# Kernel tuning notes

Measured on AMD Instinct MI355X. Metric: run time of the kernel, lower is better.

## Reference

```python
import jax, jax.numpy as jnp
import numpy as np

D = 2048
H = 16
DK = D // H
B = 2
S = 2048


def setup_inputs() -> dict:
    key = jax.random.key(0)
    ks = jax.random.split(key, 11)
    s = 1.0 / np.sqrt(D)
    inp = {
        "q": jax.random.normal(ks[0], (B, S, D), jnp.float32),
        "k": jax.random.normal(ks[1], (B, S, D), jnp.float32),
        "v": jax.random.normal(ks[2], (B, S, D), jnp.float32),
        "mask": 0,
        "Wq": jax.random.normal(ks[3], (D, D), jnp.float32) * s,
        "bq": jax.random.normal(ks[4], (D,), jnp.float32) * s,
        "Wk": jax.random.normal(ks[5], (D, D), jnp.float32) * s,
        "bk": jax.random.normal(ks[6], (D,), jnp.float32) * s,
        "Wv": jax.random.normal(ks[7], (D, D), jnp.float32) * s,
        "bv": jax.random.normal(ks[8], (D,), jnp.float32) * s,
        "Wo": jax.random.normal(ks[9], (D, D), jnp.float32) * s,
        "bo": jax.random.normal(ks[10], (D,), jnp.float32) * s,
    }
    return inp


def reference(q, k, v, mask, Wq, bq, Wk, bk, Wv, bv, Wo, bo):
    # Linear projections (torch Linear: x @ W.T + b)
    query = q @ Wq.T + bq  # [B,S,D]
    key_ = k @ Wk.T + bk
    value = v @ Wv.T + bv
    # split heads -> [B,S,H,DK]
    query = query.reshape(B, S, H, DK)
    key_ = key_.reshape(B, S, H, DK)
    value = value.reshape(B, S, H, DK)
    # scores [B,H,Sq,Sk]
    scores = jnp.einsum('nqhd,nkhd->nhqk', query, key_)
    if mask:
        # faithful to source: fill where triu(ones, diag=1) == 0 (lower tri incl diag)
        tri = jnp.triu(jnp.ones((S, S), jnp.float32), k=1)
        scores = jnp.where(tri == 0, jnp.float32(-1e20), scores)
    attn = jax.nn.softmax(scores / np.sqrt(DK), axis=3)
    # dropout=0.0 -> identity
    out = jnp.einsum('nhql,nlhd->nqhd', attn, value).reshape(B, S, D)
    return out @ Wo.T + bo
```

## Files before the change

kernel.cpp:

```cpp
#include <hip/hip_runtime.h>
#include <math.h>

typedef unsigned short u16;
typedef u16 u16x8 __attribute__((ext_vector_type(8)));
typedef u16 u16x4 __attribute__((ext_vector_type(4)));
typedef short s16x8 __attribute__((ext_vector_type(8)));
typedef short s16x4 __attribute__((ext_vector_type(4)));
typedef float f32x4 __attribute__((ext_vector_type(4)));

static constexpr int B_ = 2;
static constexpr int S_ = 2048;
static constexpr int D_ = 2048;
static constexpr int H_ = 16;
static constexpr int DK = 128;
static constexpr long long BSD = (long long)B_ * S_ * D_;
static constexpr long long DD  = (long long)D_ * D_;

#if __has_builtin(__builtin_amdgcn_mfma_f32_16x16x32_bf16)
#define HAVE_MFMA32 1
#else
#define HAVE_MFMA32 0
#endif
#if __has_builtin(__builtin_amdgcn_mfma_f32_16x16x16bf16_1k)
#define HAVE_MFMA16 1
#else
#define HAVE_MFMA16 0
#endif

__device__ __forceinline__ u16 f2bf(float f) {
    union { float f; unsigned u; } cv; cv.f = f;
    unsigned u = cv.u;
    return (u16)((u + 0x7fffu + ((u >> 16) & 1u)) >> 16);
}

__device__ __forceinline__ unsigned pack2bf(float a, float b) {
    union { float f; unsigned u; } x, y; x.f = a; y.f = b;
    return ((y.u + 0x8000u) & 0xffff0000u) | ((x.u + 0x8000u) >> 16);
}

__device__ __forceinline__ f32x4 mfma32(f32x4 c, u16x8 a, u16x8 b) {
#if HAVE_MFMA32
    return __builtin_amdgcn_mfma_f32_16x16x32_bf16((s16x8)a, (s16x8)b, c, 0, 0, 0);
#else
    asm volatile("v_mfma_f32_16x16x32_bf16 %0, %1, %2, %0" : "+v"(c) : "v"(a), "v"(b));
    return c;
#endif
}
__device__ __forceinline__ f32x4 mfma16(f32x4 c, u16x4 a, u16x4 b) {
#if HAVE_MFMA16
    return __builtin_amdgcn_mfma_f32_16x16x16bf16_1k((s16x4)a, (s16x4)b, c, 0, 0, 0);
#else
    asm volatile("v_mfma_f32_16x16x16_bf16 %0, %1, %2, %0" : "+v"(c) : "v"(a), "v"(b));
    return c;
#endif
}
__device__ __forceinline__ void fence32() {
#if !HAVE_MFMA32
    asm volatile("s_nop 7\ns_nop 7" :::);
#endif
}
__device__ __forceinline__ void fence16() {
#if !HAVE_MFMA16
    asm volatile("s_nop 7\ns_nop 7" :::);
#endif
}

__device__ __forceinline__ void glds16(const u16* g, u16* l) {
    __builtin_amdgcn_global_load_lds(
        (const __attribute__((address_space(1))) unsigned int*)g,
        (__attribute__((address_space(3))) unsigned int*)l, 16, 0, 0);
}

__device__ __forceinline__ float fexp2(float x) {
#if __has_builtin(__builtin_amdgcn_exp2f)
    return __builtin_amdgcn_exp2f(x);
#else
    return exp2f(x);
#endif
}

struct CastArgs {
    const float* src[7];
    u16* dst[7];
    int start[8];
};
__global__ __launch_bounds__(256) void cast_all(CastArgs a) {
    int g = blockIdx.x * 256 + threadIdx.x;
    if (g >= a.start[7]) return;
    int seg = 0;
#pragma unroll
    for (int i = 1; i < 7; ++i) seg += (g >= a.start[i]) ? 1 : 0;
    int idx = g - a.start[seg];
    float4 f = ((const float4*)a.src[seg])[idx];
    ushort4 o;
    o.x = f2bf(f.x); o.y = f2bf(f.y); o.z = f2bf(f.z); o.w = f2bf(f.w);
    ((ushort4*)a.dst[seg])[idx] = o;
}

__global__ __launch_bounds__(256) void transpose_v(const u16* __restrict__ V,
                                                   u16* __restrict__ Vt) {
    __shared__ u16 tile[32][33];
    int z = blockIdx.z;
    int b = z >> 4, h = z & 15;
    const u16* src = V + (long long)b * S_ * D_ + (long long)h * DK;
    u16* dst = Vt + (long long)z * DK * S_;
    int l0 = blockIdx.x * 32, d0 = blockIdx.y * 32;
    int c = threadIdx.x & 31, r0 = threadIdx.x >> 5;
#pragma unroll
    for (int i = 0; i < 4; ++i) {
        int r = r0 + i * 8;
        tile[r][c] = src[(long long)(l0 + r) * D_ + d0 + c];
    }
    __syncthreads();
#pragma unroll
    for (int i = 0; i < 4; ++i) {
        int r = r0 + i * 8;
        dst[(long long)(d0 + r) * S_ + l0 + c] = tile[c][r];
    }
}

template <typename OutT, bool BIAS>
__global__ __launch_bounds__(256) void gemm_bt(const u16* __restrict__ A,
                                               const u16* __restrict__ B,
                                               OutT* __restrict__ C,
                                               const float* __restrict__ bias,
                                               float scale) {
    __shared__ u16 SM[8192];
    u16* As = SM;
    u16* Bs = SM + 4096;

    const int t = threadIdx.x;
    const int wave = t >> 6, lane = t & 63;
    const int quad = lane >> 4, l16 = lane & 15;
    const int wm = (wave >> 1) * 64;
    const int wn = (wave & 1) * 64;
    const long long m0 = (long long)blockIdx.y * 128;
    const long long n0 = (long long)blockIdx.x * 128;

    f32x4 acc[4][4];
#pragma unroll
    for (int i = 0; i < 4; ++i)
#pragma unroll
        for (int j = 0; j < 4; ++j)
            acc[i][j] = f32x4{0.f, 0.f, 0.f, 0.f};

    for (int k0 = 0; k0 < D_; k0 += 32) {
        __syncthreads();
#pragma unroll
        for (int s = 0; s < 2; ++s) {
            int slot = s * 256 + t;
            int row = slot >> 2;
            int c = (t & 3) ^ ((row >> 1) & 3);
            glds16(A + (m0 + row) * D_ + k0 + c * 8, &As[slot * 8]);
        }
#pragma unroll
        for (int s = 0; s < 2; ++s) {
            int slot = s * 256 + t;
            int row = slot >> 2;
            int c = (t & 3) ^ ((row >> 1) & 3);
            glds16(B + (n0 + row) * D_ + k0 + c * 8, &Bs[slot * 8]);
        }
        __syncthreads();

        u16x8 af[4], bf[4];
#pragma unroll
        for (int i = 0; i < 4; ++i) {
            int row = wm + i * 16 + l16;
            af[i] = *(const u16x8*)(&As[row * 32 + ((quad ^ ((row >> 1) & 3)) * 8)]);
        }
#pragma unroll
        for (int j = 0; j < 4; ++j) {
            int row = wn + j * 16 + l16;
            bf[j] = *(const u16x8*)(&Bs[row * 32 + ((quad ^ ((row >> 1) & 3)) * 8)]);
        }
#pragma unroll
        for (int i = 0; i < 4; ++i)
#pragma unroll
            for (int j = 0; j < 4; ++j)
                acc[i][j] = mfma32(acc[i][j], af[i], bf[j]);
    }

    fence32();

    float bs[4];
#pragma unroll
    for (int j = 0; j < 4; ++j)
        bs[j] = BIAS ? bias[(int)n0 + wn + j * 16 + l16] : 0.f;

    if constexpr (sizeof(OutT) == 2) {
#pragma unroll
        for (int p = 0; p < 2; ++p) {
            __syncthreads();
#pragma unroll
            for (int jj = 0; jj < 2; ++jj) {
                int j = p * 2 + jj;
#pragma unroll
                for (int i = 0; i < 4; ++i)
#pragma unroll
                    for (int r = 0; r < 4; ++r) {
                        int row = wm + i * 16 + quad * 4 + r;
                        int lc = (wave & 1) * 32 + jj * 16 + l16;
                        SM[row * 64 + lc] = f2bf((acc[i][j][r] + bs[j]) * scale);
                    }
            }
            __syncthreads();
#pragma unroll
            for (int i = 0; i < 4; ++i) {
                int idx = i * 256 + t;
                int row = idx >> 3, cc = idx & 7;
                u16x8 val = *(const u16x8*)(&SM[row * 64 + cc * 8]);
                long long n = n0 + 32 * p + (cc & 3) * 8 + (cc >> 2) * 64;
                *(u16x8*)((u16*)C + (m0 + row) * (long long)D_ + n) = val;
            }
        }
    } else {
        float* Cf = (float*)SM;
#pragma unroll
        for (int p = 0; p < 4; ++p) {
            __syncthreads();
            int j = p;
#pragma unroll
            for (int i = 0; i < 4; ++i)
#pragma unroll
                for (int r = 0; r < 4; ++r) {
                    int row = wm + i * 16 + quad * 4 + r;
                    int lc = (wave & 1) * 16 + l16;
                    Cf[row * 32 + lc] = (acc[i][j][r] + bs[j]) * scale;
                }
            __syncthreads();
#pragma unroll
            for (int i = 0; i < 4; ++i) {
                int idx = i * 256 + t;
                int row = idx >> 3, cc = idx & 7;
                f32x4 val = *(const f32x4*)(&Cf[row * 32 + cc * 4]);
                long long n = n0 + 16 * p + (cc & 3) * 4 + (cc >> 2) * 64;
                *(f32x4*)((float*)C + (m0 + row) * (long long)D_ + n) = val;
            }
        }
    }
}

__global__ __launch_bounds__(512, 2) void flash_attn(const u16* __restrict__ Qb,
                                                     const u16* __restrict__ Kb,
                                                     const u16* __restrict__ Vt,
                                                     u16* __restrict__ Ob) {
    extern __shared__ u16 SM[];
    const int z  = blockIdx.x;
    const int qt = blockIdx.y;
    const int b  = z >> 4, h = z & 15;
    const int t = threadIdx.x, wave = t >> 6, lane = t & 63;
    const int quad = lane >> 4, l16 = lane & 15;

    u16* Ksb0 = SM;
    u16* Ksb1 = SM + 16384;
    u16* Vsb0 = SM + 32768;
    u16* Vsb1 = SM + 49152;

    const u16* kbase = Kb + (long long)(b * S_) * D_ + h * DK;
    const u16* vbase = Vt + (long long)z * DK * S_;

    u16x8 qf[2][4];
    {
        const u16* qbase = Qb + ((long long)(b * S_ + qt * 256 + wave * 32 + l16)) * D_
                              + h * DK + quad * 8;
#pragma unroll
        for (int jq = 0; jq < 2; ++jq)
#pragma unroll
            for (int kk = 0; kk < 4; ++kk)
                qf[jq][kk] = *(const u16x8*)(qbase + (long long)jq * 16 * D_ + kk * 32);
    }

    f32x4 acc_o[2][8];
#pragma unroll
    for (int jq = 0; jq < 2; ++jq)
#pragma unroll
        for (int jd = 0; jd < 8; ++jd)
            acc_o[jq][jd] = f32x4{0.f, 0.f, 0.f, 0.f};
    float m_[2] = {-3e38f, -3e38f}, l_[2] = {0.f, 0.f};

    {
#pragma unroll
        for (int i = 0; i < 4; ++i) {
            int slot = i * 512 + t;
            int row = slot >> 4;
            int cs = (slot & 15) ^ (row & 7);
            glds16(kbase + (long long)row * D_ + cs * 8, Ksb0 + slot * 8);
        }
#pragma unroll
        for (int i = 0; i < 4; ++i) {
            int slot = i * 512 + t;
            int row = slot >> 4;
            int cs = (slot & 15) ^ (row & 7);
            glds16(vbase + (long long)row * S_ + cs * 8, Vsb0 + slot * 8);
        }
    }

    for (int kt = 0; kt < S_ / 128; ++kt) {
        __syncthreads();
        const int p = kt & 1;
        const u16* ks = p ? Ksb1 : Ksb0;
        const u16* vs = p ? Vsb1 : Vsb0;
        if (kt + 1 < S_ / 128) {
            u16* kd = p ? Ksb0 : Ksb1;
            u16* vd = p ? Vsb0 : Vsb1;
            const u16* ksrc = kbase + (long long)(kt + 1) * 128 * D_;
            const u16* vsrc = vbase + (kt + 1) * 128;
#pragma unroll
            for (int i = 0; i < 4; ++i) {
                int slot = i * 512 + t;
                int row = slot >> 4;
                int cs = (slot & 15) ^ (row & 7);
                glds16(ksrc + (long long)row * D_ + cs * 8, kd + slot * 8);
            }
#pragma unroll
            for (int i = 0; i < 4; ++i) {
                int slot = i * 512 + t;
                int row = slot >> 4;
                int cs = (slot & 15) ^ (row & 7);
                glds16(vsrc + (long long)row * S_ + cs * 8, vd + slot * 8);
            }
        }

        f32x4 st[8][2];
#pragma unroll
        for (int ik = 0; ik < 8; ++ik)
#pragma unroll
            for (int jq = 0; jq < 2; ++jq)
                st[ik][jq] = f32x4{0.f, 0.f, 0.f, 0.f};
#pragma unroll
        for (int kk = 0; kk < 4; ++kk) {
            u16x8 kf[8];
#pragma unroll
            for (int ik = 0; ik < 8; ++ik) {
                int krow = ik * 16 + l16;
                kf[ik] = *(const u16x8*)(&ks[krow * 128 + (((kk * 4 + quad) ^ (l16 & 7)) * 8)]);
            }
#pragma unroll
            for (int ik = 0; ik < 8; ++ik) {
                st[ik][0] = mfma32(st[ik][0], kf[ik], qf[0][kk]);
                st[ik][1] = mfma32(st[ik][1], kf[ik], qf[1][kk]);
            }
        }
        fence32();

        float alpha[2];
#pragma unroll
        for (int jq = 0; jq < 2; ++jq) {
            float mx = st[0][jq][0];
#pragma unroll
            for (int ik = 0; ik < 8; ++ik)
#pragma unroll
                for (int r = 0; r < 4; ++r) mx = fmaxf(mx, st[ik][jq][r]);
            mx = fmaxf(mx, __shfl_xor(mx, 16, 64));
            mx = fmaxf(mx, __shfl_xor(mx, 32, 64));
            float mn = fmaxf(m_[jq], mx);
            alpha[jq] = fexp2(m_[jq] - mn);
            m_[jq] = mn;
            float sum = 0.f;
#pragma unroll
            for (int ik = 0; ik < 8; ++ik)
#pragma unroll
                for (int r = 0; r < 4; ++r) {
                    float pv = fexp2(st[ik][jq][r] - mn);
                    st[ik][jq][r] = pv;
                    sum += pv;
                }
            sum += __shfl_xor(sum, 16, 64);
            sum += __shfl_xor(sum, 32, 64);
            l_[jq] = l_[jq] * alpha[jq] + sum;
        }

        float ar[2][4];
#pragma unroll
        for (int jq = 0; jq < 2; ++jq)
#pragma unroll
            for (int r = 0; r < 4; ++r)
                ar[jq][r] = __shfl(alpha[jq], quad * 20 + r, 64);
#pragma unroll
        for (int jq = 0; jq < 2; ++jq)
#pragma unroll
            for (int jd = 0; jd < 8; ++jd)
#pragma unroll
                for (int r = 0; r < 4; ++r)
                    acc_o[jq][jd][r] *= ar[jq][r];

#pragma unroll
        for (int ik = 0; ik < 8; ++ik) {
            u16x4 pf0, pf1;
            {
                union { u16x4 v; unsigned u[2]; } pk;
                pk.u[0] = pack2bf(st[ik][0][0], st[ik][0][1]);
                pk.u[1] = pack2bf(st[ik][0][2], st[ik][0][3]);
                pf0 = pk.v;
                pk.u[0] = pack2bf(st[ik][1][0], st[ik][1][1]);
                pk.u[1] = pack2bf(st[ik][1][2], st[ik][1][3]);
                pf1 = pk.v;
            }
            const int kc = ik * 4 + quad;
            const int chi = kc >> 1, clo = kc & 1;
            u16x4 vf[8];
#pragma unroll
            for (int jd = 0; jd < 8; ++jd) {
                int vrow = jd * 16 + l16;
                vf[jd] = *(const u16x4*)(&vs[vrow * 128 + ((chi ^ (l16 & 7)) * 8) + clo * 4]);
            }
#pragma unroll
            for (int jd = 0; jd < 8; ++jd) {
                acc_o[0][jd] = mfma16(acc_o[0][jd], pf0, vf[jd]);
                acc_o[1][jd] = mfma16(acc_o[1][jd], pf1, vf[jd]);
            }
        }
        fence16();
    }

    float lr[2][4];
#pragma unroll
    for (int jq = 0; jq < 2; ++jq) {
        float inv = 1.f / l_[jq];
#pragma unroll
        for (int r = 0; r < 4; ++r)
            lr[jq][r] = __shfl(inv, quad * 20 + r, 64);
    }
    __syncthreads();
#pragma unroll
    for (int jq = 0; jq < 2; ++jq)
#pragma unroll
        for (int r = 0; r < 4; ++r) {
            int qloc = wave * 32 + jq * 16 + quad * 4 + r;
#pragma unroll
            for (int jd = 0; jd < 8; ++jd)
                SM[qloc * 128 + jd * 16 + l16] = f2bf(acc_o[jq][jd][r] * lr[jq][r]);
        }
    __syncthreads();
    u16* obase = Ob + ((long long)(b * S_ + qt * 256)) * D_ + h * DK;
#pragma unroll
    for (int i = 0; i < 8; ++i) {
        int idx = i * 512 + t;
        int row = idx >> 4, cc = idx & 15;
        *(u16x8*)(obase + (long long)row * D_ + cc * 8) = *(const u16x8*)(&SM[row * 128 + cc * 8]);
    }
}

extern "C" void kernel_launch(void* const* d_in, const int* in_sizes, int n_in,
                              void* d_out, int out_size, void* d_ws, size_t ws_size,
                              hipStream_t stream) {
    const float* q  = (const float*)d_in[0];
    const float* k  = (const float*)d_in[1];
    const float* v  = (const float*)d_in[2];
    const float* Wq = (const float*)d_in[4];
    const float* bq = (const float*)d_in[5];
    const float* Wk = (const float*)d_in[6];
    const float* bk = (const float*)d_in[7];
    const float* Wv = (const float*)d_in[8];
    const float* bv = (const float*)d_in[9];
    const float* Wo = (const float*)d_in[10];
    const float* bo = (const float*)d_in[11];
    float* out = (float*)d_out;

    u16* ws = (u16*)d_ws;
    u16* xq  = ws; ws += BSD;
    u16* xk  = ws; ws += BSD;
    u16* xv  = ws; ws += BSD;
    u16* wqb = ws; ws += DD;
    u16* wkb = ws; ws += DD;
    u16* wvb = ws; ws += DD;
    u16* wob = ws; ws += DD;
    u16* Qb  = ws; ws += BSD;
    u16* Kb  = ws; ws += BSD;
    u16* Vb  = ws; ws += BSD;
    u16* Vt  = ws; ws += BSD;
    u16* Ob  = ws; ws += BSD;

    const float q_scale = (float)(0.08838834764831845 * 1.4426950408889634);

    {
        CastArgs a;
        const float* srcs[7] = {q, k, v, Wq, Wk, Wv, Wo};
        u16* dsts[7] = {xq, xk, xv, wqb, wkb, wvb, wob};
        int n4s[7] = {(int)(BSD / 4), (int)(BSD / 4), (int)(BSD / 4),
                      (int)(DD / 4), (int)(DD / 4), (int)(DD / 4), (int)(DD / 4)};
        int acc = 0;
        for (int i = 0; i < 7; ++i) { a.src[i] = srcs[i]; a.dst[i] = dsts[i]; a.start[i] = acc; acc += n4s[i]; }
        a.start[7] = acc;
        cast_all<<<(acc + 255) / 256, 256, 0, stream>>>(a);
    }

    {
        dim3 g(D_ / 128, (B_ * S_) / 128);
        gemm_bt<u16, true><<<g, 256, 0, stream>>>(xq, wqb, Qb, bq, q_scale);
        gemm_bt<u16, true><<<g, 256, 0, stream>>>(xk, wkb, Kb, bk, 1.0f);
        gemm_bt<u16, true><<<g, 256, 0, stream>>>(xv, wvb, Vb, bv, 1.0f);
    }

    transpose_v<<<dim3(S_ / 32, DK / 32, B_ * H_), 256, 0, stream>>>(Vb, Vt);

    hipFuncSetAttribute((const void*)flash_attn,
                        hipFuncAttributeMaxDynamicSharedMemorySize, 131072);
    flash_attn<<<dim3(B_ * H_, S_ / 256), 512, 131072, stream>>>(Qb, Kb, Vt, Ob);

    {
        dim3 g(D_ / 128, (B_ * S_) / 128);
        gemm_bt<float, true><<<g, 256, 0, stream>>>(Ob, wob, out, bo, 1.0f);
    }
}
```

Baseline: 474.2 us.

## Fuse QKV projections with V transpose epilogue and retile flash attention

Merges the three QKV projection GEMMs into one launch indexed by blockIdx.z, and writes V directly in transposed per-head layout from the GEMM epilogue, which removes the separate transpose kernel and its extra buffer pass. Flash attention is retiled from 512-thread blocks with 256 queries and 128-key tiles to 256-thread blocks with 128 queries and 64-key tiles, using static shared memory. V tiles are now staged through registers, with a new swizzle, and written to LDS after the softmax step. This lowers shared memory per block and doubles the grid, trading larger tiles for more occupancy and more loop iterations.

After: 468.3 us. About the same (-1.2%).

```diff
diff --git a/kernel.cpp b/kernel.cpp
--- a/kernel.cpp
+++ b/kernel.cpp
@@ -97,37 +97,24 @@
     ((ushort4*)a.dst[seg])[idx] = o;
 }
 
-__global__ __launch_bounds__(256) void transpose_v(const u16* __restrict__ V,
-                                                   u16* __restrict__ Vt) {
-    __shared__ u16 tile[32][33];
-    int z = blockIdx.z;
-    int b = z >> 4, h = z & 15;
-    const u16* src = V + (long long)b * S_ * D_ + (long long)h * DK;
-    u16* dst = Vt + (long long)z * DK * S_;
-    int l0 = blockIdx.x * 32, d0 = blockIdx.y * 32;
-    int c = threadIdx.x & 31, r0 = threadIdx.x >> 5;
-#pragma unroll
-    for (int i = 0; i < 4; ++i) {
-        int r = r0 + i * 8;
-        tile[r][c] = src[(long long)(l0 + r) * D_ + d0 + c];
-    }
-    __syncthreads();
-#pragma unroll
-    for (int i = 0; i < 4; ++i) {
-        int r = r0 + i * 8;
-        dst[(long long)(d0 + r) * S_ + l0 + c] = tile[c][r];
-    }
-}
-
-template <typename OutT, bool BIAS>
-__global__ __launch_bounds__(256) void gemm_bt(const u16* __restrict__ A,
-                                               const u16* __restrict__ B,
-                                               OutT* __restrict__ C,
-                                               const float* __restrict__ bias,
-                                               float scale) {
-    __shared__ u16 SM[8192];
+struct QkvArgs {
+    const u16* X[3];
+    const u16* W[3];
+    const float* bias[3];
+    u16* outQ;
+    u16* outK;
+    u16* outVt;
+    float scaleQ;
+};
+__global__ __launch_bounds__(256) void qkv_proj(QkvArgs a) {
+    __shared__ u16 SM[8704];
     u16* As = SM;
     u16* Bs = SM + 4096;
+
+    const int zsel = blockIdx.z;
+    const u16* A = a.X[zsel];
+    const u16* Bw = a.W[zsel];
+    const float scale = (zsel == 0) ? a.scaleQ : 1.0f;
 
     const int t = threadIdx.x;
     const int wave = t >> 6, lane = t & 63;
@@ -158,7 +145,7 @@
             int slot = s * 256 + t;
             int row = slot >> 2;
             int c = (t & 3) ^ ((row >> 1) & 3);
-            glds16(B + (n0 + row) * D_ + k0 + c * 8, &Bs[slot * 8]);
+            glds16(Bw + (n0 + row) * D_ + k0 + c * 8, &Bs[slot * 8]);
         }
         __syncthreads();
 
@@ -185,9 +172,10 @@
     float bs[4];
 #pragma unroll
     for (int j = 0; j < 4; ++j)
-        bs[j] = BIAS ? bias[(int)n0 + wn + j * 16 + l16] : 0.f;
-
-    if constexpr (sizeof(OutT) == 2) {
+        bs[j] = a.bias[zsel][(int)n0 + wn + j * 16 + l16];
+
+    if (zsel < 2) {
+        u16* C = (zsel == 0) ? a.outQ : a.outK;
 #pragma unroll
         for (int p = 0; p < 2; ++p) {
             __syncthreads();
@@ -210,58 +198,153 @@
                 int row = idx >> 3, cc = idx & 7;
                 u16x8 val = *(const u16x8*)(&SM[row * 64 + cc * 8]);
                 long long n = n0 + 32 * p + (cc & 3) * 8 + (cc >> 2) * 64;
-                *(u16x8*)((u16*)C + (m0 + row) * (long long)D_ + n) = val;
+                *(u16x8*)(C + (m0 + row) * (long long)D_ + n) = val;
             }
         }
     } else {
-        float* Cf = (float*)SM;
-#pragma unroll
-        for (int p = 0; p < 4; ++p) {
+        const int h = blockIdx.x;
+        const int b = (int)(m0 >> 11);
+        const int tok0 = (int)(m0 & 2047);
+        const int z = b * 16 + h;
+        u16* vt = a.outVt + (long long)z * DK * S_;
+#pragma unroll
+        for (int p = 0; p < 2; ++p) {
             __syncthreads();
-            int j = p;
-#pragma unroll
-            for (int i = 0; i < 4; ++i)
-#pragma unroll
-                for (int r = 0; r < 4; ++r) {
-                    int row = wm + i * 16 + quad * 4 + r;
-                    int lc = (wave & 1) * 16 + l16;
-                    Cf[row * 32 + lc] = (acc[i][j][r] + bs[j]) * scale;
-                }
+#pragma unroll
+            for (int jj = 0; jj < 2; ++jj) {
+                int j = p * 2 + jj;
+#pragma unroll
+                for (int i = 0; i < 4; ++i)
+#pragma unroll
+                    for (int r = 0; r < 4; ++r) {
+                        int row = wm + i * 16 + quad * 4 + r;
+                        int lc = (wave & 1) * 32 + jj * 16 + l16;
+                        SM[lc * 136 + row] = f2bf(acc[i][j][r] + bs[j]);
+                    }
+            }
             __syncthreads();
 #pragma unroll
             for (int i = 0; i < 4; ++i) {
                 int idx = i * 256 + t;
-                int row = idx >> 3, cc = idx & 7;
-                f32x4 val = *(const f32x4*)(&Cf[row * 32 + cc * 4]);
-                long long n = n0 + 16 * p + (cc & 3) * 4 + (cc >> 2) * 64;
-                *(f32x4*)((float*)C + (m0 + row) * (long long)D_ + n) = val;
-            }
-        }
-    }
-}
-
-__global__ __launch_bounds__(512, 2) void flash_attn(const u16* __restrict__ Qb,
+                int lc = idx >> 4, cc = idx & 15;
+                int d = p * 32 + (lc & 31) + (lc >> 5) * 64;
+                u16x8 val = *(const u16x8*)(&SM[lc * 136 + cc * 8]);
+                *(u16x8*)(vt + (long long)d * S_ + tok0 + cc * 8) = val;
+            }
+        }
+    }
+}
+
+__global__ __launch_bounds__(256) void gemm_out(const u16* __restrict__ A,
+                                                const u16* __restrict__ B,
+                                                float* __restrict__ C,
+                                                const float* __restrict__ bias) {
+    __shared__ u16 SM[8192];
+    u16* As = SM;
+    u16* Bs = SM + 4096;
+
+    const int t = threadIdx.x;
+    const int wave = t >> 6, lane = t & 63;
+    const int quad = lane >> 4, l16 = lane & 15;
+    const int wm = (wave >> 1) * 64;
+    const int wn = (wave & 1) * 64;
+    const long long m0 = (long long)blockIdx.y * 128;
+    const long long n0 = (long long)blockIdx.x * 128;
+
+    f32x4 acc[4][4];
+#pragma unroll
+    for (int i = 0; i < 4; ++i)
+#pragma unroll
+        for (int j = 0; j < 4; ++j)
+            acc[i][j] = f32x4{0.f, 0.f, 0.f, 0.f};
+
+    for (int k0 = 0; k0 < D_; k0 += 32) {
+        __syncthreads();
+#pragma unroll
+        for (int s = 0; s < 2; ++s) {
+            int slot = s * 256 + t;
+            int row = slot >> 2;
+            int c = (t & 3) ^ ((row >> 1) & 3);
+            glds16(A + (m0 + row) * D_ + k0 + c * 8, &As[slot * 8]);
+        }
+#pragma unroll
+        for (int s = 0; s < 2; ++s) {
+            int slot = s * 256 + t;
+            int row = slot >> 2;
+            int c = (t & 3) ^ ((row >> 1) & 3);
+            glds16(B + (n0 + row) * D_ + k0 + c * 8, &Bs[slot * 8]);
+        }
+        __syncthreads();
+
+        u16x8 af[4], bf[4];
+#pragma unroll
+        for (int i = 0; i < 4; ++i) {
+            int row = wm + i * 16 + l16;
+            af[i] = *(const u16x8*)(&As[row * 32 + ((quad ^ ((row >> 1) & 3)) * 8)]);
+        }
+#pragma unroll
+        for (int j = 0; j < 4; ++j) {
+            int row = wn + j * 16 + l16;
+            bf[j] = *(const u16x8*)(&Bs[row * 32 + ((quad ^ ((row >> 1) & 3)) * 8)]);
+        }
+#pragma unroll
+        for (int i = 0; i < 4; ++i)
+#pragma unroll
+            for (int j = 0; j < 4; ++j)
+                acc[i][j] = mfma32(acc[i][j], af[i], bf[j]);
+    }
+
+    fence32();
+
+    float bs[4];
+#pragma unroll
+    for (int j = 0; j < 4; ++j)
+        bs[j] = bias[(int)n0 + wn + j * 16 + l16];
+
+    float* Cf = (float*)SM;
+#pragma unroll
+    for (int p = 0; p < 4; ++p) {
+        __syncthreads();
+        int j = p;
+#pragma unroll
+        for (int i = 0; i < 4; ++i)
+#pragma unroll
+            for (int r = 0; r < 4; ++r) {
+                int row = wm + i * 16 + quad * 4 + r;
+                int lc = (wave & 1) * 16 + l16;
+                Cf[row * 32 + lc] = acc[i][j][r] + bs[j];
+            }
+        __syncthreads();
+#pragma unroll
+        for (int i = 0; i < 4; ++i) {
+            int idx = i * 256 + t;
+            int row = idx >> 3, cc = idx & 7;
+            f32x4 val = *(const f32x4*)(&Cf[row * 32 + cc * 4]);
+            long long n = n0 + 16 * p + (cc & 3) * 4 + (cc >> 2) * 64;
+            *(f32x4*)(C + (m0 + row) * (long long)D_ + n) = val;
+        }
+    }
+}
+
+__global__ __launch_bounds__(256, 2) void flash_attn(const u16* __restrict__ Qb,
                                                      const u16* __restrict__ Kb,
                                                      const u16* __restrict__ Vt,
                                                      u16* __restrict__ Ob) {
-    extern __shared__ u16 SM[];
+    __shared__ u16 Ks[2][64 * 128];
+    __shared__ u16 Vs[2][128 * 64];
+
     const int z  = blockIdx.x;
     const int qt = blockIdx.y;
     const int b  = z >> 4, h = z & 15;
     const int t = threadIdx.x, wave = t >> 6, lane = t & 63;
     const int quad = lane >> 4, l16 = lane & 15;
 
-    u16* Ksb0 = SM;
-    u16* Ksb1 = SM + 16384;
-    u16* Vsb0 = SM + 32768;
-    u16* Vsb1 = SM + 49152;
-
     const u16* kbase = Kb + (long long)(b * S_) * D_ + h * DK;
     const u16* vbase = Vt + (long long)z * DK * S_;
 
     u16x8 qf[2][4];
     {
-        const u16* qbase = Qb + ((long long)(b * S_ + qt * 256 + wave * 32 + l16)) * D_
+        const u16* qbase = Qb + ((long long)(b * S_ + qt * 128 + wave * 32 + l16)) * D_
                               + h * DK + quad * 8;
 #pragma unroll
         for (int jq = 0; jq < 2; ++jq)
@@ -278,65 +361,75 @@
             acc_o[jq][jd] = f32x4{0.f, 0.f, 0.f, 0.f};
     float m_[2] = {-3e38f, -3e38f}, l_[2] = {0.f, 0.f};
 
+    u16x8 vreg[4];
+
     {
+        const u16* ksrc = kbase;
 #pragma unroll
         for (int i = 0; i < 4; ++i) {
-            int slot = i * 512 + t;
+            int slot = i * 256 + t;
             int row = slot >> 4;
             int cs = (slot & 15) ^ (row & 7);
-            glds16(kbase + (long long)row * D_ + cs * 8, Ksb0 + slot * 8);
+            glds16(ksrc + (long long)row * D_ + cs * 8, &Ks[0][slot * 8]);
         }
 #pragma unroll
         for (int i = 0; i < 4; ++i) {
-            int slot = i * 512 + t;
-            int row = slot >> 4;
-            int cs = (slot & 15) ^ (row & 7);
-            glds16(vbase + (long long)row * S_ + cs * 8, Vsb0 + slot * 8);
-        }
-    }
-
-    for (int kt = 0; kt < S_ / 128; ++kt) {
+            int slot = i * 256 + t;
+            int row = slot >> 3, c16 = slot & 7;
+            vreg[i] = *(const u16x8*)(vbase + (long long)row * S_ + c16 * 8);
+        }
+#pragma unroll
+        for (int i = 0; i < 4; ++i) {
+            int slot = i * 256 + t;
+            int row = slot >> 3, c16 = slot & 7;
+            int rm = row & 15;
+            u16x4 lo = __builtin_shufflevector(vreg[i], vreg[i], 0, 1, 2, 3);
+            u16x4 hi = __builtin_shufflevector(vreg[i], vreg[i], 4, 5, 6, 7);
+            *(u16x4*)(&Vs[0][row * 64 + (((2 * c16) ^ rm) * 4)]) = lo;
+            *(u16x4*)(&Vs[0][row * 64 + (((2 * c16 + 1) ^ rm) * 4)]) = hi;
+        }
+    }
+
+    for (int kt = 0; kt < S_ / 64; ++kt) {
         __syncthreads();
         const int p = kt & 1;
-        const u16* ks = p ? Ksb1 : Ksb0;
-        const u16* vs = p ? Vsb1 : Vsb0;
-        if (kt + 1 < S_ / 128) {
-            u16* kd = p ? Ksb0 : Ksb1;
-            u16* vd = p ? Vsb0 : Vsb1;
-            const u16* ksrc = kbase + (long long)(kt + 1) * 128 * D_;
-            const u16* vsrc = vbase + (kt + 1) * 128;
+        const u16* ks = Ks[p];
+        const u16* vs = Vs[p];
+        const bool pre = (kt + 1) < (S_ / 64);
+        if (pre) {
+            const u16* ksrc = kbase + (long long)(kt + 1) * 64 * D_;
 #pragma unroll
             for (int i = 0; i < 4; ++i) {
-                int slot = i * 512 + t;
+                int slot = i * 256 + t;
                 int row = slot >> 4;
                 int cs = (slot & 15) ^ (row & 7);
-                glds16(ksrc + (long long)row * D_ + cs * 8, kd + slot * 8);
-            }
+                glds16(ksrc + (long long)row * D_ + cs * 8, &Ks[p ^ 1][slot * 8]);
+            }
+            const u16* vsrc = vbase + (kt + 1) * 64;
 #pragma unroll
             for (int i = 0; i < 4; ++i) {
-                int slot = i * 512 + t;
-                int row = slot >> 4;
-                int cs = (slot & 15) ^ (row & 7);
-                glds16(vsrc + (long long)row * S_ + cs * 8, vd + slot * 8);
-            }
-        }
-
-        f32x4 st[8][2];
-#pragma unroll
-        for (int ik = 0; ik < 8; ++ik)
+                int slot = i * 256 + t;
+                int row = slot >> 3, c16 = slot & 7;
+                vreg[i] = *(const u16x8*)(vsrc + (long long)row * S_ + c16 * 8);
+            }
+        }
+
+        f32x4 st[4][2];
+#pragma unroll
+        for (int ik = 0; ik < 4; ++ik)
 #pragma unroll
             for (int jq = 0; jq < 2; ++jq)
                 st[ik][jq] = f32x4{0.f, 0.f, 0.f, 0.f};
 #pragma unroll
         for (int kk = 0; kk < 4; ++kk) {
-            u16x8 kf[8];
-#pragma unroll
-            for (int ik = 0; ik < 8; ++ik) {
+            u16x8 kf[4];
+#pragma unroll
+            for (int ik = 0; ik < 4; ++ik) {
                 int krow = ik * 16 + l16;
                 kf[ik] = *(const u16x8*)(&ks[krow * 128 + (((kk * 4 + quad) ^ (l16 & 7)) * 8)]);
             }
 #pragma unroll
-            for (int ik = 0; ik < 8; ++ik) {
+            for (int ik = 0; ik < 4; ++ik) {
                 st[ik][0] = mfma32(st[ik][0], kf[ik], qf[0][kk]);
                 st[ik][1] = mfma32(st[ik][1], kf[ik], qf[1][kk]);
             }
@@ -348,7 +441,7 @@
         for (int jq = 0; jq < 2; ++jq) {
             float mx = st[0][jq][0];
 #pragma unroll
-            for (int ik = 0; ik < 8; ++ik)
+            for (int ik = 0; ik < 4; ++ik)
 #pragma unroll
                 for (int r = 0; r < 4; ++r) mx = fmaxf(mx, st[ik][jq][r]);
             mx = fmaxf(mx, __shfl_xor(mx, 16, 64));
@@ -358,7 +451,7 @@
             m_[jq] = mn;
             float sum = 0.f;
 #pragma unroll
-            for (int ik = 0; ik < 8; ++ik)
+            for (int ik = 0; ik < 4; ++ik)
 #pragma unroll
                 for (int r = 0; r < 4; ++r) {
                     float pv = fexp2(st[ik][jq][r] - mn);
@@ -384,8 +477,21 @@
                 for (int r = 0; r < 4; ++r)
                     acc_o[jq][jd][r] *= ar[jq][r];
 
-#pragma unroll
-        for (int ik = 0; ik < 8; ++ik) {
+        if (pre) {
+#pragma unroll
+            for (int i = 0; i < 4; ++i) {
+                int slot = i * 256 + t;
+                int row = slot >> 3, c16 = slot & 7;
+                int rm = row & 15;
+                u16x4 lo = __builtin_shufflevector(vreg[i], vreg[i], 0, 1, 2, 3);
+                u16x4 hi = __builtin_shufflevector(vreg[i], vreg[i], 4, 5, 6, 7);
+                *(u16x4*)(&Vs[p ^ 1][row * 64 + (((2 * c16) ^ rm) * 4)]) = lo;
+                *(u16x4*)(&Vs[p ^ 1][row * 64 + (((2 * c16 + 1) ^ rm) * 4)]) = hi;
+            }
+        }
+
+#pragma unroll
+        for (int ik = 0; ik < 4; ++ik) {
             u16x4 pf0, pf1;
             {
                 union { u16x4 v; unsigned u[2]; } pk;
@@ -397,12 +503,11 @@
                 pf1 = pk.v;
             }
             const int kc = ik * 4 + quad;
-            const int chi = kc >> 1, clo = kc & 1;
             u16x4 vf[8];
 #pragma unroll
             for (int jd = 0; jd < 8; ++jd) {
                 int vrow = jd * 16 + l16;
-                vf[jd] = *(const u16x4*)(&vs[vrow * 128 + ((chi ^ (l16 & 7)) * 8) + clo * 4]);
+                vf[jd] = *(const u16x4*)(&vs[vrow * 64 + ((kc ^ l16) * 4)]);
             }
 #pragma unroll
             for (int jd = 0; jd < 8; ++jd) {
@@ -421,6 +526,7 @@
         for (int r = 0; r < 4; ++r)
             lr[jq][r] = __shfl(inv, quad * 20 + r, 64);
     }
+    u16* OS = (u16*)Ks;
     __syncthreads();
 #pragma unroll
     for (int jq = 0; jq < 2; ++jq)
@@ -429,15 +535,15 @@
             int qloc = wave * 32 + jq * 16 + quad * 4 + r;
 #pragma unroll
             for (int jd = 0; jd < 8; ++jd)
-                SM[qloc * 128 + jd * 16 + l16] = f2bf(acc_o[jq][jd][r] * lr[jq][r]);
+                OS[qloc * 128 + jd * 16 + l16] = f2bf(acc_o[jq][jd][r] * lr[jq][r]);
         }
     __syncthreads();
-    u16* obase = Ob + ((long long)(b * S_ + qt * 256)) * D_ + h * DK;
+    u16* obase = Ob + ((long long)(b * S_ + qt * 128)) * D_ + h * DK;
 #pragma unroll
     for (int i = 0; i < 8; ++i) {
-        int idx = i * 512 + t;
+        int idx = i * 256 + t;
         int row = idx >> 4, cc = idx & 15;
-        *(u16x8*)(obase + (long long)row * D_ + cc * 8) = *(const u16x8*)(&SM[row * 128 + cc * 8]);
+        *(u16x8*)(obase + (long long)row * D_ + cc * 8) = *(const u16x8*)(&OS[row * 128 + cc * 8]);
     }
 }
 
@@ -467,7 +573,6 @@
     u16* wob = ws; ws += DD;
     u16* Qb  = ws; ws += BSD;
     u16* Kb  = ws; ws += BSD;
-    u16* Vb  = ws; ws += BSD;
     u16* Vt  = ws; ws += BSD;
     u16* Ob  = ws; ws += BSD;
 
@@ -486,20 +591,16 @@
     }
 
     {
-        dim3 g(D_ / 128, (B_ * S_) / 128);
-        gemm_bt<u16, true><<<g, 256, 0, stream>>>(xq, wqb, Qb, bq, q_scale);
-        gemm_bt<u16, true><<<g, 256, 0, stream>>>(xk, wkb, Kb, bk, 1.0f);
-        gemm_bt<u16, true><<<g, 256, 0, stream>>>(xv, wvb, Vb, bv, 1.0f);
-    }
-
-    transpose_v<<<dim3(S_ / 32, DK / 32, B_ * H_), 256, 0, stream>>>(Vb, Vt);
-
-    hipFuncSetAttribute((const void*)flash_attn,
-                        hipFuncAttributeMaxDynamicSharedMemorySize, 131072);
-    flash_attn<<<dim3(B_ * H_, S_ / 256), 512, 131072, stream>>>(Qb, Kb, Vt, Ob);
-
-    {
-        dim3 g(D_ / 128, (B_ * S_) / 128);
-        gemm_bt<float, true><<<g, 256, 0, stream>>>(Ob, wob, out, bo, 1.0f);
-    }
-}
+        QkvArgs a;
+        a.X[0] = xq;  a.X[1] = xk;  a.X[2] = xv;
+        a.W[0] = wqb; a.W[1] = wkb; a.W[2] = wvb;
+        a.bias[0] = bq; a.bias[1] = bk; a.bias[2] = bv;
+        a.outQ = Qb; a.outK = Kb; a.outVt = Vt;
+        a.scaleQ = q_scale;
+        qkv_proj<<<dim3(D_ / 128, (B_ * S_) / 128, 3), 256, 0, stream>>>(a);
+    }
+
+    flash_attn<<<dim3(B_ * H_, S_ / 128), 256, 0, stream>>>(Qb, Kb, Vt, Ob);
+
+    gemm_out<<<dim3(D_ / 128, (B_ * S_) / 128), 256, 0, stream>>>(Ob, wob, out, bo);
+}
```
